# Optimization experiments

Measured on AMD Instinct MI355X. Metric: run time of the kernel, lower is better.

Reference implementation:

```python
import jax, jax.numpy as jnp
import numpy as np

N, F, T, C = 20000, 4, 12, 256
HID, OUT = 128, 12
ER, E = 30000, 320000


def _gcn_agg(xw, src, dst, w):
    """GCNConv propagation with self-loops (weight 1): D^-1/2 (A+I) D^-1/2 @ xw.
    xw: [N, T, C] pre-projected features; src/dst: [E] int; w: [E] edge weights."""
    n = xw.shape[0]
    deg = jnp.zeros((n,), xw.dtype).at[dst].add(w) + 1.0  # +1 from self-loop
    dinv = jax.lax.rsqrt(deg)
    coef = (dinv[src] * w * dinv[dst])[:, None, None]      # [E,1,1]
    out = jnp.zeros_like(xw).at[dst].add(coef * xw[src])   # scatter-add messages
    return out + (dinv * dinv)[:, None, None] * xw         # self-loop term


def _regional_conv(x, Wc, bc, regs):
    # Shared GCNConv applied to each of the 5 state graphs, outputs summed.
    xw = jnp.einsum("nft,fc->ntc", x, Wc)  # [N, T, C], all periods at once
    out = bc
    for (src, dst, w) in regs:
        out = out + _gcn_agg(xw, src, dst, w)
    return out


def _forward(x, attrs, idxs, Wc_z, bc_z, Wl_z, bl_z, Wc_h, bc_h, Wl_h, bl_h,
             attention, W1, b1, W2, b2):
    regs = [(idx[0], idx[1], w) for idx, w in zip(idxs, attrs)]
    # A3TGCN runs an independent TGCN-GRU step per period from H=None (zeros),
    # then attention-averages over periods. With H=0:
    #   Z = sigmoid(linear_z([conv_z(X_t), 0]))   (hidden half of Wl drops out)
    #   reset gate R multiplies H=0, so it has no effect on the output
    #   H_tilde = tanh(linear_h([conv_h(X_t), 0]));  H_t = (1-Z)*H_tilde
    cz = _regional_conv(x, Wc_z, bc_z, regs)         # [N, T, C]
    Z = jax.nn.sigmoid(cz @ Wl_z[:C] + bl_z)
    ch = _regional_conv(x, Wc_h, bc_h, regs)
    Htilde = jnp.tanh(ch @ Wl_h[:C] + bl_h)
    Ht = (1.0 - Z) * Htilde                          # [N, T, C]
    probs = jax.nn.softmax(attention)                # [T]
    h = jnp.einsum("ntc,t->nc", Ht, probs)           # temporal attention pooling
    y = jax.nn.relu(h)
    y = jax.nn.relu(y @ W1 + b1)
    y = y @ W2 + b2
    return y, h


def setup_inputs():
    key = jax.random.key(0)
    ks = jax.random.split(key, 32)
    s = 0.05
    inp = {
        "x": jax.random.normal(ks[0], (N, F, T), jnp.float32),
        "edge_index": jax.random.randint(ks[1], (2, E), 0, N, jnp.int32),
    }
    regions = ["IA", "KS", "KY", "OH", "WI"]
    for i, nm in enumerate(regions):
        inp[nm + "edge_index"] = jax.random.randint(ks[2 + i], (2, ER), 0, N, jnp.int32)
    for i, nm in enumerate(regions):
        inp[nm + "edge_attr"] = jax.random.uniform(ks[7 + i], (ER,), jnp.float32)
    for gi, g in enumerate(["z", "r", "h"]):
        inp["Wc_" + g] = jax.random.normal(ks[12 + gi], (F, C), jnp.float32) * s
        inp["bc_" + g] = jnp.zeros((C,), jnp.float32)
        inp["Wl_" + g] = jax.random.normal(ks[15 + gi], (2 * C, C), jnp.float32) * s
        inp["bl_" + g] = jnp.zeros((C,), jnp.float32)
    inp["attention"] = jax.random.normal(ks[18], (T,), jnp.float32)
    inp["W1"] = jax.random.normal(ks[19], (C, HID), jnp.float32) * s
    inp["b1"] = jnp.zeros((HID,), jnp.float32)
    inp["W2"] = jax.random.normal(ks[20], (HID, OUT), jnp.float32) * s
    inp["b2"] = jnp.zeros((OUT,), jnp.float32)
    return inp


def reference(x, edge_index, IAedge_index, KSedge_index, KYedge_index, OHedge_index, WIedge_index,
              IAedge_attr, KSedge_attr, KYedge_attr, OHedge_attr, WIedge_attr,
              Wc_z, bc_z, Wl_z, bl_z, Wc_r, bc_r, Wl_r, bl_r, Wc_h, bc_h, Wl_h, bl_h,
              attention, W1, b1, W2, b2):
    # The full-graph edge_index and the reset-gate parameters are carried by the
    # original module but cannot influence the output (regional convs use the 5
    # state graphs; the reset gate multiplies the zero initial hidden state).
    idxs = [IAedge_index, KSedge_index, KYedge_index, OHedge_index, WIedge_index]
    attrs = [IAedge_attr, KSedge_attr, KYedge_attr, OHedge_attr, WIedge_attr]
    return _forward(x, attrs, idxs, Wc_z, bc_z, Wl_z, bl_z, Wc_h, bc_h, Wl_h, bl_h,
                    attention, W1, b1, W2, b2)
```

## Files before the change

kernel.cpp:

```cpp
#include <hip/hip_runtime.h>

constexpr int N    = 20000;
constexpr int T    = 12;
constexpr int C    = 256;
constexpr int HIDN = 128;
constexpr int OUTD = 12;
constexpr int ER   = 30000;
constexpr int NFT  = 48;
constexpr int EDGE_TOT = 5 * ER;
constexpr int CAP      = 32;
constexpr int EB       = 586;

constexpr int WS_DEG    = 0;
constexpr int WS_CNT    = 100000;
constexpr int WS_MV     = 120000;
constexpr int WS_ZEND   = 122576;
constexpr int WS_WP     = 122576;
constexpr int WS_W2T    = 138960;
constexpr int WS_XV     = 140496;
constexpr int WS_BUCKET = 1100496;

constexpr float LOG2E = 1.4426950408889634f;

typedef __attribute__((ext_vector_type(8))) short short8;
typedef __attribute__((ext_vector_type(4))) float floatx4;

#if __has_builtin(__builtin_amdgcn_exp2f)
#define EXP2(x) __builtin_amdgcn_exp2f(x)
#else
#define EXP2(x) exp2f(x)
#endif

__device__ __forceinline__ short f2bf(float f) {
  unsigned u = __float_as_uint(f);
  u = u + 0x7fffu + ((u >> 16) & 1u);
  return (short)(u >> 16);
}

__device__ __forceinline__ void pick_region(
    int r,
    const int* e0, const int* e1, const int* e2, const int* e3, const int* e4,
    const float* a0, const float* a1, const float* a2, const float* a3, const float* a4,
    const int*& ei, const float*& ea) {
  switch (r) {
    case 0: ei = e0; ea = a0; break;
    case 1: ei = e1; ea = a1; break;
    case 2: ei = e2; ea = a2; break;
    case 3: ei = e3; ea = a3; break;
    default: ei = e4; ea = a4; break;
  }
}

__global__ void k_prep_deg(
    const float* __restrict__ Wc_z, const float* __restrict__ bc_z,
    const float* __restrict__ Wl_z, const float* __restrict__ bl_z,
    const float* __restrict__ Wc_h, const float* __restrict__ bc_h,
    const float* __restrict__ Wl_h, const float* __restrict__ bl_h,
    const float* __restrict__ att, const float* __restrict__ W1,
    const float* __restrict__ W2,
    const int* __restrict__ e0, const int* __restrict__ e1,
    const int* __restrict__ e2, const int* __restrict__ e3,
    const int* __restrict__ e4,
    const float* __restrict__ a0, const float* __restrict__ a1,
    const float* __restrict__ a2, const float* __restrict__ a3,
    const float* __restrict__ a4,
    float* __restrict__ Mv, short* __restrict__ Wp, float* __restrict__ W2t,
    float* __restrict__ deg) {
  int b = blockIdx.x, tid = threadIdx.x;
  if (b < 16) {
    int g  = b >> 3;
    int ch = b & 7;
    int k  = tid;
    const float* Wc = g ? Wc_h : Wc_z;
    const float* bc = g ? bc_h : bc_z;
    const float* Wl = g ? Wl_h : Wl_z;
    const float* bl = g ? bl_h : bl_z;
    float scale = g ? 2.0f * LOG2E : LOG2E;
    float m0 = 0.f, m1 = 0.f, m2 = 0.f, m3 = 0.f;
    float v = (ch == 0) ? bl[k] : 0.0f;
    int c0 = ch * 32;
    for (int c = c0; c < c0 + 32; c++) {
      float wl = Wl[c * C + k];
      m0 = fmaf(Wc[0 * C + c], wl, m0);
      m1 = fmaf(Wc[1 * C + c], wl, m1);
      m2 = fmaf(Wc[2 * C + c], wl, m2);
      m3 = fmaf(Wc[3 * C + c], wl, m3);
      v  = fmaf(bc[c], wl, v);
    }
    float* o = Mv + g * (5 * C);
    atomicAdd(&o[0 * C + k], scale * m0);
    atomicAdd(&o[1 * C + k], scale * m1);
    atomicAdd(&o[2 * C + k], scale * m2);
    atomicAdd(&o[3 * C + k], scale * m3);
    atomicAdd(&o[4 * C + k], scale * v);
    return;
  }
  if (b == 16) {
    if (tid < T) {
      float amax = -3.0e38f;
      for (int t = 0; t < T; t++) amax = fmaxf(amax, att[t]);
      float s = 0.f;
      for (int t = 0; t < T; t++) s += __expf(att[t] - amax);
      Mv[10 * C + tid] = __expf(att[tid] - amax) / s;
    }
    return;
  }
  if (b < 152) {
    int idx = (b - 17) * 256 + tid;
    if (idx < 32768) {
      int j    = idx & 7;
      int lane = (idx >> 3) & 63;
      int ch   = (idx >> 9) & 7;
      int kt   = idx >> 12;
      int cin  = ch * 32 + (lane >> 4) * 8 + j;
      int kout = kt * 16 + (lane & 15);
      Wp[idx] = f2bf(W1[cin * HIDN + kout]);
    } else if (idx < 32768 + 1536) {
      int r = idx - 32768;
      int o = r >> 7, k = r & 127;
      W2t[r] = W2[k * OUTD + o];
    }
    return;
  }
  int i = (b - 152) * 256 + tid;
  if (i >= EDGE_TOT) return;
  int r = i / ER;
  int e = i - r * ER;
  const int* ei; const float* ea;
  pick_region(r, e0, e1, e2, e3, e4, a0, a1, a2, a3, a4, ei, ea);
  atomicAdd(&deg[r * N + ei[ER + e]], ea[e]);
}

__global__ void k_fill(const int* __restrict__ e0, const int* __restrict__ e1,
                       const int* __restrict__ e2, const int* __restrict__ e3,
                       const int* __restrict__ e4,
                       const float* __restrict__ a0, const float* __restrict__ a1,
                       const float* __restrict__ a2, const float* __restrict__ a3,
                       const float* __restrict__ a4,
                       const float* __restrict__ deg, int* __restrict__ cnt,
                       int2* __restrict__ bucket) {
  int i = blockIdx.x * blockDim.x + threadIdx.x;
  if (i >= EDGE_TOT) return;
  int r = i / ER;
  int e = i - r * ER;
  const int* ei; const float* ea;
  pick_region(r, e0, e1, e2, e3, e4, a0, a1, a2, a3, a4, ei, ea);
  int src = ei[e];
  int dst = ei[ER + e];
  float cf = rsqrtf(deg[r * N + src] + 1.0f) * ea[e] * rsqrtf(deg[r * N + dst] + 1.0f);
  int slot = atomicAdd(&cnt[dst], 1);
  if (slot < CAP) bucket[dst * CAP + slot] = make_int2(src, __float_as_int(cf));
}

__global__ __launch_bounds__(256) void k_gather(
    const float* __restrict__ x, const float* __restrict__ deg,
    const int* __restrict__ cnt, const int2* __restrict__ bucket,
    float* __restrict__ xv) {
  int wave = threadIdx.x >> 6, lane = threadIdx.x & 63;
  int n = blockIdx.x * 4 + wave;
  int q = lane < NFT ? lane : NFT - 1;
  float s = 0.f;
#pragma unroll
  for (int r = 0; r < 5; r++) s += 1.0f / (deg[r * N + n] + 1.0f);
  float acc = s * x[n * NFT + q];
  int cv = cnt[n];
  if (cv > CAP) cv = CAP;
  const int2* bk = bucket + n * CAP;
  for (int j = 0; j < cv; j++) {
    int2 m = bk[j];
    acc = fmaf(__int_as_float(m.y), x[m.x * NFT + q], acc);
  }
  if (lane < NFT) xv[n * NFT + q] = acc;
}

__global__ __launch_bounds__(256) void k_gates_mlp(
    const float* __restrict__ xv, const float* __restrict__ Mv,
    const short* __restrict__ Wp, const float* __restrict__ b1,
    const float* __restrict__ W2t, const float* __restrict__ b2,
    float* __restrict__ y_out, float* __restrict__ h_out) {
  __shared__ short hs[16][264];
  __shared__ float y1s[16][132];
  int tid = threadIdx.x;
  int wave = tid >> 6, lane = tid & 63;
  int quad = lane >> 4, col = lane & 15;
  int n0 = blockIdx.x * 16;

  int c0 = lane << 2;
  const float* Mz = Mv;
  const float* Mh = Mv + 5 * C;
  float mz[4][4], mh[4][4], vz[4], vh[4];
#pragma unroll
  for (int f = 0; f < 4; f++) {
    float4 t1 = *(const float4*)(Mz + f * C + c0);
    mz[f][0] = t1.x; mz[f][1] = t1.y; mz[f][2] = t1.z; mz[f][3] = t1.w;
    float4 t2 = *(const float4*)(Mh + f * C + c0);
    mh[f][0] = t2.x; mh[f][1] = t2.y; mh[f][2] = t2.z; mh[f][3] = t2.w;
  }
  {
    float4 t1 = *(const float4*)(Mz + 4 * C + c0);
    vz[0] = t1.x; vz[1] = t1.y; vz[2] = t1.z; vz[3] = t1.w;
    float4 t2 = *(const float4*)(Mh + 4 * C + c0);
    vh[0] = t2.x; vh[1] = t2.y; vh[2] = t2.z; vh[3] = t2.w;
  }
  float p[T];
#pragma unroll
  for (int t = 0; t < T; t++) p[t] = Mv[10 * C + t];

#pragma unroll
  for (int nl = 0; nl < 4; nl++) {
    int rl = wave * 4 + nl;
    int n = n0 + rl;
    const float* xr = xv + n * NFT;
    float acc[4] = {0.f, 0.f, 0.f, 0.f};
#pragma unroll
    for (int tb = 0; tb < 3; tb++) {
      float4 xf0 = *(const float4*)(xr + 0 * T + tb * 4);
      float4 xf1 = *(const float4*)(xr + 1 * T + tb * 4);
      float4 xf2 = *(const float4*)(xr + 2 * T + tb * 4);
      float4 xf3 = *(const float4*)(xr + 3 * T + tb * 4);
      float xs0[4] = {xf0.x, xf0.y, xf0.z, xf0.w};
      float xs1[4] = {xf1.x, xf1.y, xf1.z, xf1.w};
      float xs2[4] = {xf2.x, xf2.y, xf2.z, xf2.w};
      float xs3[4] = {xf3.x, xf3.y, xf3.z, xf3.w};
#pragma unroll
      for (int tt = 0; tt < 4; tt++) {
        int t = tb * 4 + tt;
        float x0 = xs0[tt], x1 = xs1[tt], x2 = xs2[tt], x3 = xs3[tt];
#pragma unroll
        for (int j = 0; j < 4; j++) {
          float az = fmaf(mz[0][j], x0, fmaf(mz[1][j], x1, fmaf(mz[2][j], x2, fmaf(mz[3][j], x3, vz[j]))));
          float ah = fmaf(mh[0][j], x0, fmaf(mh[1][j], x1, fmaf(mh[2][j], x2, fmaf(mh[3][j], x3, vh[j]))));
          float e1 = EXP2(az);
          float e2 = EXP2(ah);
          float num = e2 - 1.0f;
          float den = (1.0f + e1) * (1.0f + e2);
          float rD  = __builtin_amdgcn_rcpf(den);
          acc[j] = fmaf(p[t] * num, rD, acc[j]);
        }
      }
    }
    float4 o = {acc[0], acc[1], acc[2], acc[3]};
    *(float4*)(h_out + n * C + c0) = o;
    unsigned lo = (unsigned short)f2bf(fmaxf(acc[0], 0.f)) |
                  ((unsigned)(unsigned short)f2bf(fmaxf(acc[1], 0.f)) << 16);
    unsigned hi = (unsigned short)f2bf(fmaxf(acc[2], 0.f)) |
                  ((unsigned)(unsigned short)f2bf(fmaxf(acc[3], 0.f)) << 16);
    *(int2*)&hs[rl][c0] = make_int2((int)lo, (int)hi);
  }
  __syncthreads();

  floatx4 acc2[2];
  acc2[0] = {0.f, 0.f, 0.f, 0.f};
  acc2[1] = {0.f, 0.f, 0.f, 0.f};
#pragma unroll
  for (int ch = 0; ch < 8; ch++) {
    short8 a = *(const short8*)&hs[col][ch * 32 + quad * 8];
#pragma unroll
    for (int kk = 0; kk < 2; kk++) {
      short8 b = ((const short8*)Wp)[((wave * 2 + kk) * 8 + ch) * 64 + lane];
      acc2[kk] = __builtin_amdgcn_mfma_f32_16x16x32_bf16(a, b, acc2[kk], 0, 0, 0);
    }
  }
#pragma unroll
  for (int kk = 0; kk < 2; kk++) {
    int kt = wave * 2 + kk;
    float bias = b1[kt * 16 + col];
#pragma unroll
    for (int r = 0; r < 4; r++)
      y1s[quad * 4 + r][kt * 16 + col] = fmaxf(acc2[kk][r] + bias, 0.f);
  }
  __syncthreads();

  if (tid < 16 * OUTD) {
    int nl = tid / OUTD, o = tid - nl * OUTD;
    float sacc = b2[o];
    const float* yr = &y1s[nl][0];
    const float* wr = W2t + o * HIDN;
#pragma unroll 8
    for (int k4 = 0; k4 < 32; k4++) {
      float4 yv = *(const float4*)(yr + 4 * k4);
      float4 wv = *(const float4*)(wr + 4 * k4);
      sacc = fmaf(yv.x, wv.x, fmaf(yv.y, wv.y, fmaf(yv.z, wv.z, fmaf(yv.w, wv.w, sacc))));
    }
    y_out[(n0 + nl) * OUTD + o] = sacc;
  }
}

extern "C" void kernel_launch(void* const* d_in, const int* in_sizes, int n_in,
                              void* d_out, int out_size, void* d_ws, size_t ws_size,
                              hipStream_t stream) {
  const float* x   = (const float*)d_in[0];
  const int* eIA = (const int*)d_in[2];
  const int* eKS = (const int*)d_in[3];
  const int* eKY = (const int*)d_in[4];
  const int* eOH = (const int*)d_in[5];
  const int* eWI = (const int*)d_in[6];
  const float* aIA = (const float*)d_in[7];
  const float* aKS = (const float*)d_in[8];
  const float* aKY = (const float*)d_in[9];
  const float* aOH = (const float*)d_in[10];
  const float* aWI = (const float*)d_in[11];
  const float* Wc_z = (const float*)d_in[12];
  const float* bc_z = (const float*)d_in[13];
  const float* Wl_z = (const float*)d_in[14];
  const float* bl_z = (const float*)d_in[15];
  const float* Wc_h = (const float*)d_in[20];
  const float* bc_h = (const float*)d_in[21];
  const float* Wl_h = (const float*)d_in[22];
  const float* bl_h = (const float*)d_in[23];
  const float* att  = (const float*)d_in[24];
  const float* W1   = (const float*)d_in[25];
  const float* b1   = (const float*)d_in[26];
  const float* W2   = (const float*)d_in[27];
  const float* b2   = (const float*)d_in[28];

  float* ws     = (float*)d_ws;
  float* deg    = ws + WS_DEG;
  int*   cnt    = (int*)(ws + WS_CNT);
  float* Mv     = ws + WS_MV;
  short* Wp     = (short*)(ws + WS_WP);
  float* W2t    = ws + WS_W2T;
  float* xvb    = ws + WS_XV;
  int2*  bucket = (int2*)(ws + WS_BUCKET);

  float* y_out = (float*)d_out;
  float* h_out = y_out + N * OUTD;

  hipMemsetAsync(deg, 0, WS_ZEND * sizeof(float), stream);

  k_prep_deg<<<152 + EB, 256, 0, stream>>>(Wc_z, bc_z, Wl_z, bl_z,
                                           Wc_h, bc_h, Wl_h, bl_h,
                                           att, W1, W2,
                                           eIA, eKS, eKY, eOH, eWI,
                                           aIA, aKS, aKY, aOH, aWI,
                                           Mv, Wp, W2t, deg);
  k_fill<<<EB, 256, 0, stream>>>(eIA, eKS, eKY, eOH, eWI,
                                 aIA, aKS, aKY, aOH, aWI,
                                 deg, cnt, bucket);
  k_gather<<<N / 4, 256, 0, stream>>>(x, deg, cnt, bucket, xvb);
  k_gates_mlp<<<N / 16, 256, 0, stream>>>(xvb, Mv, Wp, b1, W2t, b2, y_out, h_out);
}
```

Measured before the change: 202.4 us.

## Fuse neighbor gather with gate computation and split MLP into separate kernel

Moves the gate/tanh/attention-pooling math into the gather kernel: each wave keeps its aggregated 48 features in registers and broadcasts them via lane shuffles, so the xv intermediate buffer is no longer written and read back. The MLP becomes its own kernel that reloads h from the output buffer, converts it to bf16 and runs the MFMA layers. This saves the xv round trip but adds a reread of h (20000x256 floats) and changes per-block work partitioning for the gate math.

Result: slower. 210.6 us (+4.0%).

```diff
diff --git a/kernel.cpp b/kernel.cpp
--- a/kernel.cpp
+++ b/kernel.cpp
@@ -17,8 +17,7 @@
 constexpr int WS_ZEND   = 122576;
 constexpr int WS_WP     = 122576;
 constexpr int WS_W2T    = 138960;
-constexpr int WS_XV     = 140496;
-constexpr int WS_BUCKET = 1100496;
+constexpr int WS_BUCKET = 140496;
 
 constexpr float LOG2E = 1.4426950408889634f;
 
@@ -152,99 +151,88 @@
   if (slot < CAP) bucket[dst * CAP + slot] = make_int2(src, __float_as_int(cf));
 }
 
-__global__ __launch_bounds__(256) void k_gather(
+__global__ __launch_bounds__(256) void k_gather_gates(
     const float* __restrict__ x, const float* __restrict__ deg,
     const int* __restrict__ cnt, const int2* __restrict__ bucket,
-    float* __restrict__ xv) {
+    const float* __restrict__ Mv, float* __restrict__ h_out) {
   int wave = threadIdx.x >> 6, lane = threadIdx.x & 63;
   int n = blockIdx.x * 4 + wave;
+
   int q = lane < NFT ? lane : NFT - 1;
   float s = 0.f;
 #pragma unroll
   for (int r = 0; r < 5; r++) s += 1.0f / (deg[r * N + n] + 1.0f);
-  float acc = s * x[n * NFT + q];
+  float facc = s * x[n * NFT + q];
   int cv = cnt[n];
   if (cv > CAP) cv = CAP;
   const int2* bk = bucket + n * CAP;
   for (int j = 0; j < cv; j++) {
     int2 m = bk[j];
-    acc = fmaf(__int_as_float(m.y), x[m.x * NFT + q], acc);
-  }
-  if (lane < NFT) xv[n * NFT + q] = acc;
-}
-
-__global__ __launch_bounds__(256) void k_gates_mlp(
-    const float* __restrict__ xv, const float* __restrict__ Mv,
-    const short* __restrict__ Wp, const float* __restrict__ b1,
-    const float* __restrict__ W2t, const float* __restrict__ b2,
-    float* __restrict__ y_out, float* __restrict__ h_out) {
+    facc = fmaf(__int_as_float(m.y), x[m.x * NFT + q], facc);
+  }
+
+  int c0 = lane << 2;
+  const float* Mz = Mv;
+  const float* Mh = Mv + 5 * C;
+  float mz[4][4], mh[4][4], vz[4], vh[4];
+#pragma unroll
+  for (int f = 0; f < 4; f++) {
+    float4 t1 = *(const float4*)(Mz + f * C + c0);
+    mz[f][0] = t1.x; mz[f][1] = t1.y; mz[f][2] = t1.z; mz[f][3] = t1.w;
+    float4 t2 = *(const float4*)(Mh + f * C + c0);
+    mh[f][0] = t2.x; mh[f][1] = t2.y; mh[f][2] = t2.z; mh[f][3] = t2.w;
+  }
+  {
+    float4 t1 = *(const float4*)(Mz + 4 * C + c0);
+    vz[0] = t1.x; vz[1] = t1.y; vz[2] = t1.z; vz[3] = t1.w;
+    float4 t2 = *(const float4*)(Mh + 4 * C + c0);
+    vh[0] = t2.x; vh[1] = t2.y; vh[2] = t2.z; vh[3] = t2.w;
+  }
+
+  float acc[4] = {0.f, 0.f, 0.f, 0.f};
+#pragma unroll
+  for (int t = 0; t < T; t++) {
+    float p  = Mv[10 * C + t];
+    float x0 = __shfl(facc, t);
+    float x1 = __shfl(facc, T + t);
+    float x2 = __shfl(facc, 2 * T + t);
+    float x3 = __shfl(facc, 3 * T + t);
+#pragma unroll
+    for (int j = 0; j < 4; j++) {
+      float az = fmaf(mz[0][j], x0, fmaf(mz[1][j], x1, fmaf(mz[2][j], x2, fmaf(mz[3][j], x3, vz[j]))));
+      float ah = fmaf(mh[0][j], x0, fmaf(mh[1][j], x1, fmaf(mh[2][j], x2, fmaf(mh[3][j], x3, vh[j]))));
+      float e1 = EXP2(az);
+      float e2 = EXP2(ah);
+      float num = e2 - 1.0f;
+      float den = (1.0f + e1) * (1.0f + e2);
+      float rD  = __builtin_amdgcn_rcpf(den);
+      acc[j] = fmaf(p * num, rD, acc[j]);
+    }
+  }
+  float4 o = {acc[0], acc[1], acc[2], acc[3]};
+  *(float4*)(h_out + n * C + c0) = o;
+}
+
+__global__ __launch_bounds__(256) void k_mlp16(
+    const float* __restrict__ h_in, const short* __restrict__ Wp,
+    const float* __restrict__ b1, const float* __restrict__ W2t,
+    const float* __restrict__ b2, float* __restrict__ y_out) {
   __shared__ short hs[16][264];
   __shared__ float y1s[16][132];
   int tid = threadIdx.x;
   int wave = tid >> 6, lane = tid & 63;
   int quad = lane >> 4, col = lane & 15;
   int n0 = blockIdx.x * 16;
-
   int c0 = lane << 2;
-  const float* Mz = Mv;
-  const float* Mh = Mv + 5 * C;
-  float mz[4][4], mh[4][4], vz[4], vh[4];
-#pragma unroll
-  for (int f = 0; f < 4; f++) {
-    float4 t1 = *(const float4*)(Mz + f * C + c0);
-    mz[f][0] = t1.x; mz[f][1] = t1.y; mz[f][2] = t1.z; mz[f][3] = t1.w;
-    float4 t2 = *(const float4*)(Mh + f * C + c0);
-    mh[f][0] = t2.x; mh[f][1] = t2.y; mh[f][2] = t2.z; mh[f][3] = t2.w;
-  }
-  {
-    float4 t1 = *(const float4*)(Mz + 4 * C + c0);
-    vz[0] = t1.x; vz[1] = t1.y; vz[2] = t1.z; vz[3] = t1.w;
-    float4 t2 = *(const float4*)(Mh + 4 * C + c0);
-    vh[0] = t2.x; vh[1] = t2.y; vh[2] = t2.z; vh[3] = t2.w;
-  }
-  float p[T];
-#pragma unroll
-  for (int t = 0; t < T; t++) p[t] = Mv[10 * C + t];
 
 #pragma unroll
   for (int nl = 0; nl < 4; nl++) {
     int rl = wave * 4 + nl;
-    int n = n0 + rl;
-    const float* xr = xv + n * NFT;
-    float acc[4] = {0.f, 0.f, 0.f, 0.f};
-#pragma unroll
-    for (int tb = 0; tb < 3; tb++) {
-      float4 xf0 = *(const float4*)(xr + 0 * T + tb * 4);
-      float4 xf1 = *(const float4*)(xr + 1 * T + tb * 4);
-      float4 xf2 = *(const float4*)(xr + 2 * T + tb * 4);
-      float4 xf3 = *(const float4*)(xr + 3 * T + tb * 4);
-      float xs0[4] = {xf0.x, xf0.y, xf0.z, xf0.w};
-      float xs1[4] = {xf1.x, xf1.y, xf1.z, xf1.w};
-      float xs2[4] = {xf2.x, xf2.y, xf2.z, xf2.w};
-      float xs3[4] = {xf3.x, xf3.y, xf3.z, xf3.w};
-#pragma unroll
-      for (int tt = 0; tt < 4; tt++) {
-        int t = tb * 4 + tt;
-        float x0 = xs0[tt], x1 = xs1[tt], x2 = xs2[tt], x3 = xs3[tt];
-#pragma unroll
-        for (int j = 0; j < 4; j++) {
-          float az = fmaf(mz[0][j], x0, fmaf(mz[1][j], x1, fmaf(mz[2][j], x2, fmaf(mz[3][j], x3, vz[j]))));
-          float ah = fmaf(mh[0][j], x0, fmaf(mh[1][j], x1, fmaf(mh[2][j], x2, fmaf(mh[3][j], x3, vh[j]))));
-          float e1 = EXP2(az);
-          float e2 = EXP2(ah);
-          float num = e2 - 1.0f;
-          float den = (1.0f + e1) * (1.0f + e2);
-          float rD  = __builtin_amdgcn_rcpf(den);
-          acc[j] = fmaf(p[t] * num, rD, acc[j]);
-        }
-      }
-    }
-    float4 o = {acc[0], acc[1], acc[2], acc[3]};
-    *(float4*)(h_out + n * C + c0) = o;
-    unsigned lo = (unsigned short)f2bf(fmaxf(acc[0], 0.f)) |
-                  ((unsigned)(unsigned short)f2bf(fmaxf(acc[1], 0.f)) << 16);
-    unsigned hi = (unsigned short)f2bf(fmaxf(acc[2], 0.f)) |
-                  ((unsigned)(unsigned short)f2bf(fmaxf(acc[3], 0.f)) << 16);
+    float4 hv = *(const float4*)(h_in + (n0 + rl) * C + c0);
+    unsigned lo = (unsigned short)f2bf(fmaxf(hv.x, 0.f)) |
+                  ((unsigned)(unsigned short)f2bf(fmaxf(hv.y, 0.f)) << 16);
+    unsigned hi = (unsigned short)f2bf(fmaxf(hv.z, 0.f)) |
+                  ((unsigned)(unsigned short)f2bf(fmaxf(hv.w, 0.f)) << 16);
     *(int2*)&hs[rl][c0] = make_int2((int)lo, (int)hi);
   }
   __syncthreads();
@@ -320,7 +308,6 @@
   float* Mv     = ws + WS_MV;
   short* Wp     = (short*)(ws + WS_WP);
   float* W2t    = ws + WS_W2T;
-  float* xvb    = ws + WS_XV;
   int2*  bucket = (int2*)(ws + WS_BUCKET);
 
   float* y_out = (float*)d_out;
@@ -337,6 +324,6 @@
   k_fill<<<EB, 256, 0, stream>>>(eIA, eKS, eKY, eOH, eWI,
                                  aIA, aKS, aKY, aOH, aWI,
                                  deg, cnt, bucket);
-  k_gather<<<N / 4, 256, 0, stream>>>(x, deg, cnt, bucket, xvb);
-  k_gates_mlp<<<N / 16, 256, 0, stream>>>(xvb, Mv, Wp, b1, W2t, b2, y_out, h_out);
-}
+  k_gather_gates<<<N / 4, 256, 0, stream>>>(x, deg, cnt, bucket, Mv, h_out);
+  k_mlp16<<<N / 16, 256, 0, stream>>>(h_out, Wp, b1, W2t, b2, y_out);
+}
```

## Split gates and MLP into separate kernels, shuffle bucket entries in gather

Applied to the files above, without the earlier changes.

The fused gates+MLP kernel is split in two. The new gates kernel gives each node's 256 channels to two waves at two channels per lane, which spreads the exp-heavy gate math over 8x more blocks. A separate MLP kernel then re-reads h from global memory. The gather kernel now loads the node's bucket entries once per wave and broadcasts them with shuffles instead of issuing a scalar load per edge. The cost is an extra launch and an extra round-trip of h (N x 256 floats) through memory.

After: 212.4 us. 4.9% more time.

```diff
diff --git a/kernel.cpp b/kernel.cpp
--- a/kernel.cpp
+++ b/kernel.cpp
@@ -162,89 +162,96 @@
   float s = 0.f;
 #pragma unroll
   for (int r = 0; r < 5; r++) s += 1.0f / (deg[r * N + n] + 1.0f);
-  float acc = s * x[n * NFT + q];
+  float facc = s * x[n * NFT + q];
   int cv = cnt[n];
   if (cv > CAP) cv = CAP;
-  const int2* bk = bucket + n * CAP;
+  int2 mreg = bucket[n * CAP + (lane & (CAP - 1))];
   for (int j = 0; j < cv; j++) {
-    int2 m = bk[j];
-    acc = fmaf(__int_as_float(m.y), x[m.x * NFT + q], acc);
-  }
-  if (lane < NFT) xv[n * NFT + q] = acc;
-}
-
-__global__ __launch_bounds__(256) void k_gates_mlp(
+    int   src = __shfl(mreg.x, j);
+    float cf  = __int_as_float(__shfl(mreg.y, j));
+    facc = fmaf(cf, x[src * NFT + q], facc);
+  }
+  if (lane < NFT) xv[n * NFT + q] = facc;
+}
+
+__global__ __launch_bounds__(256) void k_gates(
     const float* __restrict__ xv, const float* __restrict__ Mv,
-    const short* __restrict__ Wp, const float* __restrict__ b1,
-    const float* __restrict__ W2t, const float* __restrict__ b2,
-    float* __restrict__ y_out, float* __restrict__ h_out) {
+    float* __restrict__ h_out) {
+  int wave = threadIdx.x >> 6, lane = threadIdx.x & 63;
+  int n = blockIdx.x * 2 + (wave >> 1);
+  int half = wave & 1;
+  int c0 = half * 128 + (lane << 1);
+  const float* Mz = Mv;
+  const float* Mh = Mv + 5 * C;
+  float mz[4][2], mh[4][2], vz[2], vh[2];
+#pragma unroll
+  for (int f = 0; f < 4; f++) {
+    float2 t1 = *(const float2*)(Mz + f * C + c0);
+    mz[f][0] = t1.x; mz[f][1] = t1.y;
+    float2 t2 = *(const float2*)(Mh + f * C + c0);
+    mh[f][0] = t2.x; mh[f][1] = t2.y;
+  }
+  {
+    float2 t1 = *(const float2*)(Mz + 4 * C + c0);
+    vz[0] = t1.x; vz[1] = t1.y;
+    float2 t2 = *(const float2*)(Mh + 4 * C + c0);
+    vh[0] = t2.x; vh[1] = t2.y;
+  }
+
+  const float* xr = xv + n * NFT;
+  float acc[2] = {0.f, 0.f};
+#pragma unroll
+  for (int tb = 0; tb < 3; tb++) {
+    float4 xf0 = *(const float4*)(xr + 0 * T + tb * 4);
+    float4 xf1 = *(const float4*)(xr + 1 * T + tb * 4);
+    float4 xf2 = *(const float4*)(xr + 2 * T + tb * 4);
+    float4 xf3 = *(const float4*)(xr + 3 * T + tb * 4);
+    float xs0[4] = {xf0.x, xf0.y, xf0.z, xf0.w};
+    float xs1[4] = {xf1.x, xf1.y, xf1.z, xf1.w};
+    float xs2[4] = {xf2.x, xf2.y, xf2.z, xf2.w};
+    float xs3[4] = {xf3.x, xf3.y, xf3.z, xf3.w};
+#pragma unroll
+    for (int tt = 0; tt < 4; tt++) {
+      int t = tb * 4 + tt;
+      float p = Mv[10 * C + t];
+      float x0 = xs0[tt], x1 = xs1[tt], x2 = xs2[tt], x3 = xs3[tt];
+#pragma unroll
+      for (int j = 0; j < 2; j++) {
+        float az = fmaf(mz[0][j], x0, fmaf(mz[1][j], x1, fmaf(mz[2][j], x2, fmaf(mz[3][j], x3, vz[j]))));
+        float ah = fmaf(mh[0][j], x0, fmaf(mh[1][j], x1, fmaf(mh[2][j], x2, fmaf(mh[3][j], x3, vh[j]))));
+        float e1 = EXP2(az);
+        float e2 = EXP2(ah);
+        float den = (1.0f + e1) * (1.0f + e2);
+        float rD  = __builtin_amdgcn_rcpf(den);
+        float pn  = fmaf(p, e2, -p);
+        acc[j] = fmaf(pn, rD, acc[j]);
+      }
+    }
+  }
+  float2 o = {acc[0], acc[1]};
+  *(float2*)(h_out + n * C + c0) = o;
+}
+
+__global__ __launch_bounds__(256) void k_mlp16(
+    const float* __restrict__ h_in, const short* __restrict__ Wp,
+    const float* __restrict__ b1, const float* __restrict__ W2t,
+    const float* __restrict__ b2, float* __restrict__ y_out) {
   __shared__ short hs[16][264];
   __shared__ float y1s[16][132];
   int tid = threadIdx.x;
   int wave = tid >> 6, lane = tid & 63;
   int quad = lane >> 4, col = lane & 15;
   int n0 = blockIdx.x * 16;
-
   int c0 = lane << 2;
-  const float* Mz = Mv;
-  const float* Mh = Mv + 5 * C;
-  float mz[4][4], mh[4][4], vz[4], vh[4];
-#pragma unroll
-  for (int f = 0; f < 4; f++) {
-    float4 t1 = *(const float4*)(Mz + f * C + c0);
-    mz[f][0] = t1.x; mz[f][1] = t1.y; mz[f][2] = t1.z; mz[f][3] = t1.w;
-    float4 t2 = *(const float4*)(Mh + f * C + c0);
-    mh[f][0] = t2.x; mh[f][1] = t2.y; mh[f][2] = t2.z; mh[f][3] = t2.w;
-  }
-  {
-    float4 t1 = *(const float4*)(Mz + 4 * C + c0);
-    vz[0] = t1.x; vz[1] = t1.y; vz[2] = t1.z; vz[3] = t1.w;
-    float4 t2 = *(const float4*)(Mh + 4 * C + c0);
-    vh[0] = t2.x; vh[1] = t2.y; vh[2] = t2.z; vh[3] = t2.w;
-  }
-  float p[T];
-#pragma unroll
-  for (int t = 0; t < T; t++) p[t] = Mv[10 * C + t];
 
 #pragma unroll
   for (int nl = 0; nl < 4; nl++) {
     int rl = wave * 4 + nl;
-    int n = n0 + rl;
-    const float* xr = xv + n * NFT;
-    float acc[4] = {0.f, 0.f, 0.f, 0.f};
-#pragma unroll
-    for (int tb = 0; tb < 3; tb++) {
-      float4 xf0 = *(const float4*)(xr + 0 * T + tb * 4);
-      float4 xf1 = *(const float4*)(xr + 1 * T + tb * 4);
-      float4 xf2 = *(const float4*)(xr + 2 * T + tb * 4);
-      float4 xf3 = *(const float4*)(xr + 3 * T + tb * 4);
-      float xs0[4] = {xf0.x, xf0.y, xf0.z, xf0.w};
-      float xs1[4] = {xf1.x, xf1.y, xf1.z, xf1.w};
-      float xs2[4] = {xf2.x, xf2.y, xf2.z, xf2.w};
-      float xs3[4] = {xf3.x, xf3.y, xf3.z, xf3.w};
-#pragma unroll
-      for (int tt = 0; tt < 4; tt++) {
-        int t = tb * 4 + tt;
-        float x0 = xs0[tt], x1 = xs1[tt], x2 = xs2[tt], x3 = xs3[tt];
-#pragma unroll
-        for (int j = 0; j < 4; j++) {
-          float az = fmaf(mz[0][j], x0, fmaf(mz[1][j], x1, fmaf(mz[2][j], x2, fmaf(mz[3][j], x3, vz[j]))));
-          float ah = fmaf(mh[0][j], x0, fmaf(mh[1][j], x1, fmaf(mh[2][j], x2, fmaf(mh[3][j], x3, vh[j]))));
-          float e1 = EXP2(az);
-          float e2 = EXP2(ah);
-          float num = e2 - 1.0f;
-          float den = (1.0f + e1) * (1.0f + e2);
-          float rD  = __builtin_amdgcn_rcpf(den);
-          acc[j] = fmaf(p[t] * num, rD, acc[j]);
-        }
-      }
-    }
-    float4 o = {acc[0], acc[1], acc[2], acc[3]};
-    *(float4*)(h_out + n * C + c0) = o;
-    unsigned lo = (unsigned short)f2bf(fmaxf(acc[0], 0.f)) |
-                  ((unsigned)(unsigned short)f2bf(fmaxf(acc[1], 0.f)) << 16);
-    unsigned hi = (unsigned short)f2bf(fmaxf(acc[2], 0.f)) |
-                  ((unsigned)(unsigned short)f2bf(fmaxf(acc[3], 0.f)) << 16);
+    float4 hv = *(const float4*)(h_in + (n0 + rl) * C + c0);
+    unsigned lo = (unsigned short)f2bf(fmaxf(hv.x, 0.f)) |
+                  ((unsigned)(unsigned short)f2bf(fmaxf(hv.y, 0.f)) << 16);
+    unsigned hi = (unsigned short)f2bf(fmaxf(hv.z, 0.f)) |
+                  ((unsigned)(unsigned short)f2bf(fmaxf(hv.w, 0.f)) << 16);
     *(int2*)&hs[rl][c0] = make_int2((int)lo, (int)hi);
   }
   __syncthreads();
@@ -338,5 +345,6 @@
                                  aIA, aKS, aKY, aOH, aWI,
                                  deg, cnt, bucket);
   k_gather<<<N / 4, 256, 0, stream>>>(x, deg, cnt, bucket, xvb);
-  k_gates_mlp<<<N / 16, 256, 0, stream>>>(xvb, Mv, Wp, b1, W2t, b2, y_out, h_out);
-}
+  k_gates<<<N / 2, 256, 0, stream>>>(xvb, Mv, h_out);
+  k_mlp16<<<N / 16, 256, 0, stream>>>(h_out, Wp, b1, W2t, b2, y_out);
+}
```
